# Optimization experiments

Hardware: AMD Instinct MI355X
Metric: run time of the kernel (lower is better)

## Reference

```python
import jax, jax.numpy as jnp
import numpy as np

B, H, W, C = 16, 32, 32, 256
N = H * W


def setup_inputs() -> dict:
    key = jax.random.key(0)
    ks = jax.random.split(key, 8)
    x = jax.random.normal(ks[0], (B, H, W, C), dtype=jnp.float32)
    # nn.LazyLinear(C): weight (C, C), bias (C,)
    scale = 1.0 / np.sqrt(C)
    Wq = jax.random.uniform(ks[1], (C, C), jnp.float32, -scale, scale)
    bq = jax.random.uniform(ks[2], (C,), jnp.float32, -scale, scale)
    Wk = jax.random.uniform(ks[3], (C, C), jnp.float32, -scale, scale)
    bk = jax.random.uniform(ks[4], (C,), jnp.float32, -scale, scale)
    Wv = jax.random.uniform(ks[5], (C, C), jnp.float32, -scale, scale)
    bv = jax.random.uniform(ks[6], (C,), jnp.float32, -scale, scale)
    # torch.randn(H, H*W, W)
    Wp = jax.random.normal(ks[7], (H, N, W), dtype=jnp.float32)
    return {"x": x, "Wq": Wq, "bq": bq, "Wk": Wk, "bk": bk,
            "Wv": Wv, "bv": bv, "Wp": Wp}


def reference(x, Wq, bq, Wk, bk, Wv, bv, Wp):
    b, h, w, c = x.shape
    n = h * w
    # Linear projections (torch Linear: x @ W^T + b), flatten spatial dims to N tokens
    q = (jnp.einsum('bhwc,dc->bhwd', x, Wq) + bq).reshape(b, n, c)
    k = (jnp.einsum('bhwc,dc->bhwd', x, Wk) + bk).reshape(b, n, c)
    v = (jnp.einsum('bhwc,dc->bhwd', x, Wv) + bv).reshape(b, n, c)
    # Unscaled attention over the N spatial tokens (no 1/sqrt(C) in the original)
    scores = jnp.einsum('bnc,bmc->bnm', q, k)          # (B, N, N)
    attn = jax.nn.softmax(scores, axis=-1)
    qkv = jnp.einsum('bnm,bmc->bnc', attn, v)           # (B, N, C)
    # z = (qkv^T [B,1,C,N] @ Wp [H,N,W]).transpose(-2,-1) -> (B, H, W, C)
    z = jnp.einsum('bnc,hnw->bhwc', qkv, Wp)
    return z
```

## Files before the change

kernel.cpp:

```cpp
#include <hip/hip_runtime.h>
#include <hip/hip_bf16.h>

#define BB 16
#define NN 1024
#define CC 256

typedef __attribute__((ext_vector_type(8))) short bf16x8;
typedef __attribute__((ext_vector_type(4))) float f32x4;

#define GPTR(p) ((const __attribute__((address_space(1))) void*)(p))
#define LPTR(p) ((__attribute__((address_space(3))) void*)(p))

__device__ __forceinline__ unsigned short f2bf(float f) {
  union { float f; unsigned u; } v; v.f = f;
  unsigned r = v.u + 0x7FFFu + ((v.u >> 16) & 1u);
  return (unsigned short)(r >> 16);
}

__global__ void cast_all(const float* __restrict__ x,
                         const float* __restrict__ Wq, const float* __restrict__ Wk,
                         const float* __restrict__ Wv,
                         const float* __restrict__ bq, const float* __restrict__ bk,
                         const float* __restrict__ bv,
                         unsigned short* __restrict__ xb,
                         unsigned short* __restrict__ wqkvb,
                         float* __restrict__ bqkv) {
  const int NX = BB * NN * CC;
  const int NW = CC * CC;
  int i = blockIdx.x * blockDim.x + threadIdx.x;
  if (i < NX) { xb[i] = f2bf(x[i]); return; }
  int j = i - NX;
  if (j < 3 * NW) {
    const float* w = (j < NW) ? Wq : (j < 2 * NW ? Wk : Wv);
    wqkvb[j] = f2bf(w[j % NW]);
    return;
  }
  int jj = j - 3 * NW;
  if (jj < 3 * CC) {
    const float* bb = (jj < CC) ? bq : (jj < 2 * CC ? bk : bv);
    bqkv[jj] = bb[jj % CC];
  }
}

__global__ __launch_bounds__(256) void wp_transpose(const float* __restrict__ Wp,
                                                    unsigned short* __restrict__ Amat) {
  __shared__ float tile[32][33];
  int h = blockIdx.y;
  int n0 = blockIdx.x * 32;
#pragma unroll
  for (int j = 0; j < 4; j++) {
    int idx = threadIdx.x + j * 256;
    int a = idx >> 5, wc = idx & 31;
    tile[a][wc] = Wp[(size_t)h * (NN * 32) + (size_t)(n0 + a) * 32 + wc];
  }
  __syncthreads();
#pragma unroll
  for (int j = 0; j < 4; j++) {
    int idx = threadIdx.x + j * 256;
    int wc = idx >> 5, a = idx & 31;
    Amat[(size_t)(h * 32 + wc) * NN + n0 + a] = f2bf(tile[a][wc]);
  }
}

template <int BIAS_MODE, int F32OUT>
__global__ __launch_bounds__(256) void gemm_tile(
    const unsigned short* __restrict__ A, int lda, long sA,
    const unsigned short* __restrict__ Bt, int ldb, long sB,
    const float* __restrict__ bias,
    void* __restrict__ Out, int ldo, long sO, int K) {
  __shared__ unsigned short As[2 * 128 * 32];
  __shared__ unsigned short Bs[2 * 64 * 32];
  int b = blockIdx.z;
  int m0 = blockIdx.x * 128;
  int n0 = blockIdx.y * 64;
  int t = threadIdx.x;
  int w = t >> 6, lane = t & 63;
  int wm = (w >> 1) * 64, wn = (w & 1) * 32;
  int r = lane & 15, g = lane >> 4;

  const unsigned short* Ab = A + (long)b * sA;
  const unsigned short* Bb = Bt + (long)b * sB;

  int srow = t >> 2;
  int scol = (t & 3) * 8;

  f32x4 acc[4][2];
#pragma unroll
  for (int i = 0; i < 4; i++)
#pragma unroll
    for (int j = 0; j < 2; j++) acc[i][j] = (f32x4){0.f, 0.f, 0.f, 0.f};

  for (int k0 = 0; k0 < K; k0 += 64) {
    __syncthreads();
#pragma unroll
    for (int kh = 0; kh < 2; kh++) {
#pragma unroll
      for (int jj = 0; jj < 2; jj++) {
        __builtin_amdgcn_global_load_lds(
            GPTR(Ab + (long)(m0 + srow + jj * 64) * lda + k0 + kh * 32 + scol),
            LPTR(&As[kh * 4096 + jj * 2048 + t * 8]), 16, 0, 0);
      }
      __builtin_amdgcn_global_load_lds(
          GPTR(Bb + (long)(n0 + srow) * ldb + k0 + kh * 32 + scol),
          LPTR(&Bs[kh * 2048 + t * 8]), 16, 0, 0);
    }
    __syncthreads();
#pragma unroll
    for (int kh = 0; kh < 2; kh++) {
      bf16x8 af[4], bfr[2];
#pragma unroll
      for (int ti = 0; ti < 4; ti++)
        af[ti] = *(const bf16x8*)&As[kh * 4096 + (wm + ti * 16 + r) * 32 + g * 8];
#pragma unroll
      for (int tj = 0; tj < 2; tj++)
        bfr[tj] = *(const bf16x8*)&Bs[kh * 2048 + (wn + tj * 16 + r) * 32 + g * 8];
#pragma unroll
      for (int ti = 0; ti < 4; ti++)
#pragma unroll
        for (int tj = 0; tj < 2; tj++)
          acc[ti][tj] = __builtin_amdgcn_mfma_f32_16x16x32_bf16(af[ti], bfr[tj], acc[ti][tj], 0, 0, 0);
    }
  }

#pragma unroll
  for (int ti = 0; ti < 4; ti++) {
#pragma unroll
    for (int tj = 0; tj < 2; tj++) {
      int col = n0 + wn + tj * 16 + r;
      float bc = (BIAS_MODE == 1) ? bias[col] : 0.0f;
#pragma unroll
      for (int rr = 0; rr < 4; rr++) {
        int row = m0 + wm + ti * 16 + g * 4 + rr;
        float val = acc[ti][tj][rr] + bc;
        long oidx = (long)b * sO + (long)row * ldo + col;
        if (F32OUT)
          ((float*)Out)[oidx] = val;
        else
          ((unsigned short*)Out)[oidx] = f2bf(val);
      }
    }
  }
}

__global__ __launch_bounds__(256) void gemm_qkv(
    const unsigned short* __restrict__ A,
    const unsigned short* __restrict__ Bt,
    const float* __restrict__ bias,
    unsigned short* __restrict__ Qb, unsigned short* __restrict__ Kb,
    unsigned short* __restrict__ Vtb) {
  __shared__ unsigned short As[2 * 128 * 32];
  __shared__ unsigned short Bs[2 * 64 * 32];
  int b = blockIdx.z;
  int m0 = blockIdx.x * 128;
  int n0 = blockIdx.y * 64;
  int t = threadIdx.x;
  int w = t >> 6, lane = t & 63;
  int wm = (w >> 1) * 64, wn = (w & 1) * 32;
  int r = lane & 15, g = lane >> 4;

  const unsigned short* Ab = A + (long)b * NN * CC;
  int srow = t >> 2;
  int scol = (t & 3) * 8;

  f32x4 acc[4][2];
#pragma unroll
  for (int i = 0; i < 4; i++)
#pragma unroll
    for (int j = 0; j < 2; j++) acc[i][j] = (f32x4){0.f, 0.f, 0.f, 0.f};

  for (int k0 = 0; k0 < CC; k0 += 64) {
    __syncthreads();
#pragma unroll
    for (int kh = 0; kh < 2; kh++) {
#pragma unroll
      for (int jj = 0; jj < 2; jj++) {
        __builtin_amdgcn_global_load_lds(
            GPTR(Ab + (long)(m0 + srow + jj * 64) * CC + k0 + kh * 32 + scol),
            LPTR(&As[kh * 4096 + jj * 2048 + t * 8]), 16, 0, 0);
      }
      __builtin_amdgcn_global_load_lds(
          GPTR(Bt + (long)(n0 + srow) * CC + k0 + kh * 32 + scol),
          LPTR(&Bs[kh * 2048 + t * 8]), 16, 0, 0);
    }
    __syncthreads();
#pragma unroll
    for (int kh = 0; kh < 2; kh++) {
      bf16x8 af[4], bfr[2];
#pragma unroll
      for (int ti = 0; ti < 4; ti++)
        af[ti] = *(const bf16x8*)&As[kh * 4096 + (wm + ti * 16 + r) * 32 + g * 8];
#pragma unroll
      for (int tj = 0; tj < 2; tj++)
        bfr[tj] = *(const bf16x8*)&Bs[kh * 2048 + (wn + tj * 16 + r) * 32 + g * 8];
#pragma unroll
      for (int ti = 0; ti < 4; ti++)
#pragma unroll
        for (int tj = 0; tj < 2; tj++)
          acc[ti][tj] = __builtin_amdgcn_mfma_f32_16x16x32_bf16(af[ti], bfr[tj], acc[ti][tj], 0, 0, 0);
    }
  }

  int seg = n0 >> 8;
  unsigned short* QK = (seg == 0) ? Qb : Kb;
#pragma unroll
  for (int ti = 0; ti < 4; ti++) {
#pragma unroll
    for (int tj = 0; tj < 2; tj++) {
      int col = n0 + wn + tj * 16 + r;
      int c = col & 255;
      float bc = bias[col];
#pragma unroll
      for (int rr = 0; rr < 4; rr++) {
        int row = m0 + wm + ti * 16 + g * 4 + rr;
        float val = acc[ti][tj][rr] + bc;
        if (seg < 2)
          QK[(long)b * NN * CC + (long)row * CC + c] = f2bf(val);
        else
          Vtb[(long)b * NN * CC + (long)c * NN + row] = f2bf(val);
      }
    }
  }
}

__global__ __launch_bounds__(512, 4) void attn_fused(
    const unsigned short* __restrict__ Q,
    const unsigned short* __restrict__ Km,
    const unsigned short* __restrict__ Vt,
    unsigned short* __restrict__ QKVt) {
  __shared__ unsigned short ShBuf[32 * 1024];
  __shared__ float red[4][2][16];
  int b = blockIdx.y;
  int n0 = blockIdx.x * 32;
  int t = threadIdx.x;
  int w = t >> 6, lane = t & 63;
  int rg = w >> 2, ch = w & 3;
  int r = lane & 15, g = lane >> 4;

  const unsigned short* qbase = Q + ((long)b * NN + n0 + rg * 16 + r) * CC + g * 8;
  bf16x8 qf[8];
#pragma unroll
  for (int kk = 0; kk < 8; kk++) qf[kk] = *(const bf16x8*)(qbase + kk * 32);

  const unsigned short* kbase = Km + (long)b * NN * CC;
  int strow = t >> 2;
  int stcol = (t & 3) * 8;

  f32x4 acc[16];
#pragma unroll
  for (int tt = 0; tt < 16; tt++) acc[tt] = (f32x4){0.f, 0.f, 0.f, 0.f};

  for (int kk = 0; kk < 8; kk++) {
    __syncthreads();
#pragma unroll
    for (int jj = 0; jj < 8; jj++) {
      __builtin_amdgcn_global_load_lds(
          GPTR(kbase + (long)(strow + jj * 128) * CC + kk * 32 + stcol),
          LPTR(&ShBuf[(strow + jj * 128) * 32 + stcol]), 16, 0, 0);
    }
    __syncthreads();
#pragma unroll
    for (int tt = 0; tt < 16; tt++) {
      bf16x8 bv = *(const bf16x8*)&ShBuf[(ch * 256 + tt * 16 + r) * 32 + g * 8];
      acc[tt] = __builtin_amdgcn_mfma_f32_16x16x32_bf16(qf[kk], bv, acc[tt], 0, 0, 0);
    }
  }

  float mrow[4];
#pragma unroll
  for (int rr = 0; rr < 4; rr++) {
    float m = acc[0][rr];
#pragma unroll
    for (int tt = 1; tt < 16; tt++) m = fmaxf(m, acc[tt][rr]);
#pragma unroll
    for (int d = 1; d < 16; d <<= 1) m = fmaxf(m, __shfl_xor(m, d, 64));
    mrow[rr] = m;
  }
  if (r == 0) {
#pragma unroll
    for (int rr = 0; rr < 4; rr++) red[ch][rg][g * 4 + rr] = mrow[rr];
  }
  __syncthreads();
#pragma unroll
  for (int rr = 0; rr < 4; rr++) {
    float m = red[0][rg][g * 4 + rr];
#pragma unroll
    for (int c2 = 1; c2 < 4; c2++) m = fmaxf(m, red[c2][rg][g * 4 + rr]);
    mrow[rr] = m;
  }
  __syncthreads();
  float ssum[4];
#pragma unroll
  for (int rr = 0; rr < 4; rr++) {
    float s = 0.f;
#pragma unroll
    for (int tt = 0; tt < 16; tt++) {
      float e = exp2f((acc[tt][rr] - mrow[rr]) * 1.44269504088896f);
      acc[tt][rr] = e;
      s += e;
    }
#pragma unroll
    for (int d = 1; d < 16; d <<= 1) s += __shfl_xor(s, d, 64);
    ssum[rr] = s;
  }
  if (r == 0) {
#pragma unroll
    for (int rr = 0; rr < 4; rr++) red[ch][rg][g * 4 + rr] = ssum[rr];
  }
  __syncthreads();
#pragma unroll
  for (int rr = 0; rr < 4; rr++) {
    float s = red[0][rg][g * 4 + rr] + red[1][rg][g * 4 + rr] +
              red[2][rg][g * 4 + rr] + red[3][rg][g * 4 + rr];
    float inv = 1.0f / s;
    int prow = rg * 16 + g * 4 + rr;
    int sw = prow & 7;
#pragma unroll
    for (int tt = 0; tt < 16; tt++) {
      int col = ch * 256 + tt * 16 + r;
      int chunk = (col >> 3) ^ sw;
      ShBuf[prow * 1024 + chunk * 8 + (col & 7)] = f2bf(acc[tt][rr] * inv);
    }
  }
  __syncthreads();

  const unsigned short* vbase = Vt + (long)b * NN * CC;
  int cw = w * 32;
  f32x4 o[2][2];
#pragma unroll
  for (int i = 0; i < 2; i++)
#pragma unroll
    for (int j = 0; j < 2; j++) o[i][j] = (f32x4){0.f, 0.f, 0.f, 0.f};

#pragma unroll 4
  for (int m0 = 0; m0 < NN; m0 += 32) {
    bf16x8 ar[2], br[2];
#pragma unroll
    for (int bt = 0; bt < 2; bt++)
      br[bt] = *(const bf16x8*)(vbase + (long)(cw + bt * 16 + r) * NN + m0 + g * 8);
#pragma unroll
    for (int rt = 0; rt < 2; rt++) {
      int prow = rt * 16 + r;
      int chunk = ((m0 >> 3) + g) ^ (prow & 7);
      ar[rt] = *(const bf16x8*)&ShBuf[prow * 1024 + chunk * 8];
    }
#pragma unroll
    for (int rt = 0; rt < 2; rt++)
#pragma unroll
      for (int bt = 0; bt < 2; bt++)
        o[rt][bt] = __builtin_amdgcn_mfma_f32_16x16x32_bf16(ar[rt], br[bt], o[rt][bt], 0, 0, 0);
  }

  unsigned short* obase = QKVt + (long)b * NN * CC;
#pragma unroll
  for (int rt = 0; rt < 2; rt++) {
#pragma unroll
    for (int bt = 0; bt < 2; bt++) {
      int c = cw + bt * 16 + r;
#pragma unroll
      for (int rr = 0; rr < 4; rr++) {
        int n = n0 + rt * 16 + g * 4 + rr;
        obase[(long)c * NN + n] = f2bf(o[rt][bt][rr]);
      }
    }
  }
}

extern "C" void kernel_launch(void* const* d_in, const int* in_sizes, int n_in,
                              void* d_out, int out_size, void* d_ws, size_t ws_size,
                              hipStream_t stream) {
  const float* x  = (const float*)d_in[0];
  const float* Wq = (const float*)d_in[1];
  const float* bq = (const float*)d_in[2];
  const float* Wk = (const float*)d_in[3];
  const float* bk = (const float*)d_in[4];
  const float* Wv = (const float*)d_in[5];
  const float* bv = (const float*)d_in[6];
  const float* Wp = (const float*)d_in[7];
  float* out = (float*)d_out;

  const long BNC = (long)BB * NN * CC;

  char* p = (char*)d_ws;
  unsigned short* xb    = (unsigned short*)p; p += BNC * 2;
  unsigned short* wqkvb = (unsigned short*)p; p += 3L * CC * CC * 2;
  float*          bqkv  = (float*)p;          p += 4096;
  unsigned short* Amat  = (unsigned short*)p; p += (long)NN * NN * 2;
  unsigned short* Qb    = (unsigned short*)p; p += BNC * 2;
  unsigned short* Kb    = (unsigned short*)p; p += BNC * 2;
  unsigned short* Vtb   = (unsigned short*)p; p += BNC * 2;
  unsigned short* QKVt  = (unsigned short*)p; p += BNC * 2;

  const long TOT = BNC + 3L * CC * CC + 3 * CC;
  cast_all<<<(int)((TOT + 255) / 256), 256, 0, stream>>>(
      x, Wq, Wk, Wv, bq, bk, bv, xb, wqkvb, bqkv);
  wp_transpose<<<dim3(NN / 32, 32), 256, 0, stream>>>(Wp, Amat);

  gemm_qkv<<<dim3(8, 12, BB), 256, 0, stream>>>(xb, wqkvb, bqkv, Qb, Kb, Vtb);

  attn_fused<<<dim3(NN / 32, BB), 512, 0, stream>>>(Qb, Kb, Vtb, QKVt);

  gemm_tile<0, 1><<<dim3(8, 4, BB), 256, 0, stream>>>(
      Amat, NN, 0L, QKVt, NN, (long)NN * CC, nullptr,
      out, CC, (long)NN * CC, NN);
}
```

Before: 181.0 us.

## Load K directly from global in attention and reorder grid with batch fastest

The attention kernel stops staging K tiles through LDS with global_load_lds plus two barriers per k-step. Each wave now reads its K fragments straight from global memory into registers and feeds them to MFMA. All three GEMM/attention launches swap grid dimensions so the batch index varies fastest, which changes which blocks run concurrently and how K/V and weights are shared in L2 across XCDs. The P-tile swizzle is simplified to a row-group based XOR and the PV loop unroll is reduced; the trade-off is more global/L2 traffic for K and possibly worse cache locality per batch.

Result: slower. 220.5 us (+21.8%).

```diff
diff --git a/kernel.cpp b/kernel.cpp
--- a/kernel.cpp
+++ b/kernel.cpp
@@ -70,9 +70,9 @@
     void* __restrict__ Out, int ldo, long sO, int K) {
   __shared__ unsigned short As[2 * 128 * 32];
   __shared__ unsigned short Bs[2 * 64 * 32];
-  int b = blockIdx.z;
-  int m0 = blockIdx.x * 128;
-  int n0 = blockIdx.y * 64;
+  int b = blockIdx.x;
+  int m0 = blockIdx.y * 128;
+  int n0 = blockIdx.z * 64;
   int t = threadIdx.x;
   int w = t >> 6, lane = t & 63;
   int wm = (w >> 1) * 64, wn = (w & 1) * 32;
@@ -150,9 +150,9 @@
     unsigned short* __restrict__ Vtb) {
   __shared__ unsigned short As[2 * 128 * 32];
   __shared__ unsigned short Bs[2 * 64 * 32];
-  int b = blockIdx.z;
-  int m0 = blockIdx.x * 128;
-  int n0 = blockIdx.y * 64;
+  int b = blockIdx.x;
+  int m0 = blockIdx.y * 128;
+  int n0 = blockIdx.z * 64;
   int t = threadIdx.x;
   int w = t >> 6, lane = t & 63;
   int wm = (w >> 1) * 64, wn = (w & 1) * 32;
@@ -227,10 +227,10 @@
     const unsigned short* __restrict__ Km,
     const unsigned short* __restrict__ Vt,
     unsigned short* __restrict__ QKVt) {
-  __shared__ unsigned short ShBuf[32 * 1024];
+  __shared__ unsigned short Ps[32 * 1024];
   __shared__ float red[4][2][16];
-  int b = blockIdx.y;
-  int n0 = blockIdx.x * 32;
+  int b = blockIdx.x;
+  int n0 = blockIdx.y * 32;
   int t = threadIdx.x;
   int w = t >> 6, lane = t & 63;
   int rg = w >> 2, ch = w & 3;
@@ -241,27 +241,22 @@
 #pragma unroll
   for (int kk = 0; kk < 8; kk++) qf[kk] = *(const bf16x8*)(qbase + kk * 32);
 
-  const unsigned short* kbase = Km + (long)b * NN * CC;
-  int strow = t >> 2;
-  int stcol = (t & 3) * 8;
+  const unsigned short* kb = Km + ((long)b * NN + ch * 256 + r) * CC + g * 8;
 
   f32x4 acc[16];
 #pragma unroll
   for (int tt = 0; tt < 16; tt++) acc[tt] = (f32x4){0.f, 0.f, 0.f, 0.f};
 
   for (int kk = 0; kk < 8; kk++) {
-    __syncthreads();
-#pragma unroll
-    for (int jj = 0; jj < 8; jj++) {
-      __builtin_amdgcn_global_load_lds(
-          GPTR(kbase + (long)(strow + jj * 128) * CC + kk * 32 + stcol),
-          LPTR(&ShBuf[(strow + jj * 128) * 32 + stcol]), 16, 0, 0);
-    }
-    __syncthreads();
-#pragma unroll
-    for (int tt = 0; tt < 16; tt++) {
-      bf16x8 bv = *(const bf16x8*)&ShBuf[(ch * 256 + tt * 16 + r) * 32 + g * 8];
-      acc[tt] = __builtin_amdgcn_mfma_f32_16x16x32_bf16(qf[kk], bv, acc[tt], 0, 0, 0);
+#pragma unroll
+    for (int gq = 0; gq < 4; gq++) {
+      bf16x8 kv[4];
+#pragma unroll
+      for (int i = 0; i < 4; i++)
+        kv[i] = *(const bf16x8*)(kb + (long)(gq * 4 + i) * 16 * CC + kk * 32);
+#pragma unroll
+      for (int i = 0; i < 4; i++)
+        acc[gq * 4 + i] = __builtin_amdgcn_mfma_f32_16x16x32_bf16(qf[kk], kv[i], acc[gq * 4 + i], 0, 0, 0);
     }
   }
 
@@ -313,12 +308,12 @@
               red[2][rg][g * 4 + rr] + red[3][rg][g * 4 + rr];
     float inv = 1.0f / s;
     int prow = rg * 16 + g * 4 + rr;
-    int sw = prow & 7;
+    int sw = ((prow >> 2) & 3) << 1;
 #pragma unroll
     for (int tt = 0; tt < 16; tt++) {
       int col = ch * 256 + tt * 16 + r;
       int chunk = (col >> 3) ^ sw;
-      ShBuf[prow * 1024 + chunk * 8 + (col & 7)] = f2bf(acc[tt][rr] * inv);
+      Ps[prow * 1024 + chunk * 8 + (col & 7)] = f2bf(acc[tt][rr] * inv);
     }
   }
   __syncthreads();
@@ -331,7 +326,8 @@
 #pragma unroll
     for (int j = 0; j < 2; j++) o[i][j] = (f32x4){0.f, 0.f, 0.f, 0.f};
 
-#pragma unroll 4
+  int swr = ((r >> 2) & 3) << 1;
+#pragma unroll 2
   for (int m0 = 0; m0 < NN; m0 += 32) {
     bf16x8 ar[2], br[2];
 #pragma unroll
@@ -340,8 +336,8 @@
 #pragma unroll
     for (int rt = 0; rt < 2; rt++) {
       int prow = rt * 16 + r;
-      int chunk = ((m0 >> 3) + g) ^ (prow & 7);
-      ar[rt] = *(const bf16x8*)&ShBuf[prow * 1024 + chunk * 8];
+      int chunk = ((m0 >> 3) + g) ^ swr;
+      ar[rt] = *(const bf16x8*)&Ps[prow * 1024 + chunk * 8];
     }
 #pragma unroll
     for (int rt = 0; rt < 2; rt++)
@@ -395,11 +391,11 @@
       x, Wq, Wk, Wv, bq, bk, bv, xb, wqkvb, bqkv);
   wp_transpose<<<dim3(NN / 32, 32), 256, 0, stream>>>(Wp, Amat);
 
-  gemm_qkv<<<dim3(8, 12, BB), 256, 0, stream>>>(xb, wqkvb, bqkv, Qb, Kb, Vtb);
-
-  attn_fused<<<dim3(NN / 32, BB), 512, 0, stream>>>(Qb, Kb, Vtb, QKVt);
-
-  gemm_tile<0, 1><<<dim3(8, 4, BB), 256, 0, stream>>>(
+  gemm_qkv<<<dim3(BB, 8, 12), 256, 0, stream>>>(xb, wqkvb, bqkv, Qb, Kb, Vtb);
+
+  attn_fused<<<dim3(BB, NN / 32), 512, 0, stream>>>(Qb, Kb, Vtb, QKVt);
+
+  gemm_tile<0, 1><<<dim3(BB, 8, 4), 256, 0, stream>>>(
       Amat, NN, 0L, QKVt, NN, (long)NN * CC, nullptr,
       out, CC, (long)NN * CC, NN);
 }
```
